# Kernel tuning notes

Hardware: AMD Instinct MI355X
Metric: run time of the kernel (lower is better)

Reference implementation:

```python
import jax, jax.numpy as jnp
import numpy as np


def _nn_idx(query, ref):
    """Index of nearest ref point for each query point.
    query: [B,N,3], ref: [B,M,3] -> idx [B,N] (int32).
    Squared distance via ||q||^2 - 2 q.r + ||r||^2 (matches cdist+top1).
    """
    d2 = (jnp.sum(query * query, axis=-1, keepdims=True)
          - 2.0 * jnp.einsum('bnd,bmd->bnm', query, ref)
          + jnp.sum(ref * ref, axis=-1)[:, None, :])
    return jnp.argmin(d2, axis=-1)


def setup_inputs() -> dict:
    key = jax.random.key(0)
    k1, k2, k3 = jax.random.split(key, 3)
    B, N, M = 1, 16384, 16384  # batch hard-coded to 1 in original loops
    pred = jax.random.normal(k1, (B, N, 3), dtype=jnp.float32)
    gt = jax.random.normal(k2, (B, M, 3), dtype=jnp.float32)
    weight = jax.random.uniform(k3, (1,), dtype=jnp.float32)
    return {"pred": pred, "gt": gt, "weight": weight}


def reference(pred, gt, weight):
    # get_mse_loss2: weighted bidirectional nearest-neighbor MSE.
    w = weight[0]
    # B2A: align each pred point to its nearest gt point
    idx = _nn_idx(pred, gt)                                   # [B,N]
    align_gt = jnp.take_along_axis(gt, idx[..., None], axis=1)  # [B,N,3]
    B2A = jnp.mean((pred - align_gt) ** 2)
    # A2B: align each gt point to its nearest pred point
    idx2 = _nn_idx(gt, pred)                                  # [B,M]
    align_out = jnp.take_along_axis(pred, idx2[..., None], axis=1)  # [B,M,3]
    A2B = jnp.mean((align_out - gt) ** 2)
    return B2A * w + A2B * (1.0 - w)
```

## Files before the change

### kernel.cpp

```cpp
#include <hip/hip_runtime.h>


#define NPTS   16384
#define QBLK   128
#define QCH    (NPTS / QBLK)
#define SSPLIT 4
#define RBLK   (NPTS / SSPLIT)
#define NB1    (2 * QCH * SSPLIT)

typedef __attribute__((ext_vector_type(8)))  __bf16 bf16x8;
typedef __attribute__((ext_vector_type(16))) float  floatx16;

union frag16 { __bf16 v[16]; uint4 q[2]; };

__device__ __forceinline__ float vmin16(floatx16 v) {
    float a = fminf(fminf(v[0], v[1]), v[2]);
    float b = fminf(fminf(v[3], v[4]), v[5]);
    float c = fminf(fminf(v[6], v[7]), v[8]);
    float d = fminf(fminf(v[9], v[10]), v[11]);
    float e = fminf(fminf(v[12], v[13]), fminf(v[14], v[15]));
    return fminf(fminf(fminf(a, b), fminf(c, d)), e);
}

__global__ __launch_bounds__(256) void prep_kernel(
    const float* __restrict__ pred, const float* __restrict__ gt,
    uint4* __restrict__ aform, uint4* __restrict__ bform,
    float* __restrict__ out)
{
    const int i = blockIdx.x * 256 + threadIdx.x;
    if (i == 0) out[0] = 0.0f;
    const int role = (i < NPTS) ? 0 : 1;
    const int p = i - role * NPTS;
    const float* __restrict__ src = role ? gt : pred;

    const float x = src[p * 3 + 0], y = src[p * 3 + 1], z = src[p * 3 + 2];
    const float nn = x * x + y * y + z * z;
    const __bf16 xh = (__bf16)x, yh = (__bf16)y, zh = (__bf16)z;
    const __bf16 xl = (__bf16)(x - (float)xh);
    const __bf16 yl = (__bf16)(y - (float)yh);
    const __bf16 zl = (__bf16)(z - (float)zh);
    const __bf16 nh = (__bf16)nn;
    const __bf16 nl = (__bf16)(nn - (float)nh);
    const __bf16 one = (__bf16)1.0f;

    frag16 A;
    A.v[0]  = (__bf16)(-2.0f * (float)xh); A.v[1]  = A.v[0];
    A.v[2]  = (__bf16)(-2.0f * (float)xl); A.v[3]  = A.v[2];
    A.v[4]  = (__bf16)(-2.0f * (float)yh); A.v[5]  = A.v[4];
    A.v[6]  = (__bf16)(-2.0f * (float)yl); A.v[7]  = A.v[6];
    A.v[8]  = (__bf16)(-2.0f * (float)zh); A.v[9]  = A.v[8];
    A.v[10] = (__bf16)(-2.0f * (float)zl); A.v[11] = A.v[10];
    A.v[12] = nh;  A.v[13] = nl;  A.v[14] = one;  A.v[15] = one;

    frag16 B;
    B.v[0] = xh;  B.v[1]  = xl;  B.v[2]  = xh;  B.v[3]  = xl;
    B.v[4] = yh;  B.v[5]  = yl;  B.v[6]  = yh;  B.v[7]  = yl;
    B.v[8] = zh;  B.v[9]  = zl;  B.v[10] = zh;  B.v[11] = zl;
    B.v[12] = one; B.v[13] = one; B.v[14] = nh;  B.v[15] = nl;

    uint4* da = aform + (size_t)role * (NPTS * 2)
              + ((p >> 5) * 64 + (p & 31));
    da[0]  = A.q[0];
    da[32] = A.q[1];
    uint4* db = bform + (size_t)role * (NPTS * 2) + p * 2;
    db[0] = B.q[0];
    db[1] = B.q[1];
}

__global__ __launch_bounds__(256) void nn_part_kernel(
    const uint4* __restrict__ aform, const uint4* __restrict__ bform,
    float* __restrict__ partial)
{
    const int bx   = blockIdx.x;
    const int dir  = bx >> 9;
    const int qc   = (bx & 511) >> 2;
    const int s    = bx & 3;
    const int tid  = threadIdx.x;
    const int lane = tid & 63;
    const int wave = tid >> 6;
    const int lid  = lane & 31;
    const int half = lane >> 5;

    const uint4* __restrict__ Aref = aform + (size_t)(dir ? 0 : 1) * (NPTS * 2);
    const uint4* __restrict__ Bqry = bform + (size_t)(dir ? 1 : 0) * (NPTS * 2);

    const int qbase = qc * QBLK + wave * 32;
    const bf16x8 bq = __builtin_bit_cast(bf16x8, Bqry[(qbase + lid) * 2 + half]);

    floatx16 zero;
#pragma unroll
    for (int k = 0; k < 16; ++k) zero[k] = 0.0f;
    floatx16 mnv;
#pragma unroll
    for (int k = 0; k < 16; ++k) mnv[k] = 3.4e38f;

    const uint4* gp = Aref + (size_t)s * (RBLK * 2) + half * 32 + lid;
#pragma unroll 4
    for (int t = 0; t < RBLK / 32; t += 2) {
        const bf16x8 a0 = __builtin_bit_cast(bf16x8, gp[t * 64]);
        const bf16x8 a1 = __builtin_bit_cast(bf16x8, gp[t * 64 + 64]);
        floatx16 d0 = __builtin_amdgcn_mfma_f32_32x32x16_bf16(a0, bq, zero, 0, 0, 0);
        floatx16 d1 = __builtin_amdgcn_mfma_f32_32x32x16_bf16(a1, bq, zero, 0, 0, 0);
#pragma unroll
        for (int k = 0; k < 16; ++k)
            mnv[k] = fminf(fminf(mnv[k], d0[k]), d1[k]);
    }

    float v = vmin16(mnv);
    v = fminf(v, __shfl_xor(v, 32));
    if (half == 0) {
        float* pout = partial + ((size_t)((dir * QCH + qc) * SSPLIT + s)) * QBLK
                    + wave * 32;
        pout[lid] = v;
    }
}

__global__ __launch_bounds__(QBLK) void nn_combine_kernel(
    const float* __restrict__ partial, const float* __restrict__ weight,
    float* __restrict__ out)
{
    const int b   = blockIdx.x;
    const int dir = b >> 7;
    const int qc  = b & 127;
    const int t   = threadIdx.x;

    const float* p = partial + ((size_t)((dir * QCH + qc) * SSPLIT)) * QBLK;
    float v = p[t];
#pragma unroll
    for (int s = 1; s < SSPLIT; ++s)
        v = fminf(v, p[s * QBLK + t]);

    for (int off = 32; off; off >>= 1) v += __shfl_down(v, off);
    __shared__ float ws[2];
    if ((t & 63) == 0) ws[t >> 6] = v;
    __syncthreads();
    if (t == 0) {
        const float sum = ws[0] + ws[1];
        const float wgt = weight[0];
        const float scale = (dir ? (1.0f - wgt) : wgt) / (3.0f * (float)NPTS);
        atomicAdd(out, sum * scale);
    }
}

extern "C" void kernel_launch(void* const* d_in, const int* in_sizes, int n_in,
                              void* d_out, int out_size, void* d_ws, size_t ws_size,
                              hipStream_t stream) {
    const float* pred   = (const float*)d_in[0];
    const float* gt     = (const float*)d_in[1];
    const float* weight = (const float*)d_in[2];

    float* partial = (float*)d_ws;
    uint4* aform = (uint4*)((char*)d_ws + (size_t)2 * QCH * SSPLIT * QBLK * 4);
    uint4* bform = aform + (size_t)2 * NPTS * 2;

    prep_kernel<<<2 * NPTS / 256, 256, 0, stream>>>(pred, gt, aform, bform,
                                                    (float*)d_out);
    nn_part_kernel<<<NB1, 256, 0, stream>>>(aform, bform, partial);
    nn_combine_kernel<<<2 * QCH, QBLK, 0, stream>>>(partial, weight, (float*)d_out);
}
```

Baseline: 92.68 us.

## Give each wave two query tiles and fuse MFMA with min3 in inline asm

Each wave now handles 64 query points with two B fragments, so every loaded reference A fragment feeds four MFMAs instead of two. The query block grows to 256 and the reference split to 8, which keeps the grid at 1024 blocks, and the combine kernel is resized to match. The MFMA-plus-min reduction is written in inline assembly using v_min3 on hard-coded clobbered registers v32–v63, with s_nop padding for the MFMA result hazard. The fixed nops may stall more than needed, and the hard register clobbers can constrain register allocation.

```diff
diff --git a/kernel.cpp b/kernel.cpp
--- a/kernel.cpp
+++ b/kernel.cpp
@@ -2,9 +2,9 @@
 
 
 #define NPTS   16384
-#define QBLK   128
+#define QBLK   256
 #define QCH    (NPTS / QBLK)
-#define SSPLIT 4
+#define SSPLIT 8
 #define RBLK   (NPTS / SSPLIT)
 #define NB1    (2 * QCH * SSPLIT)
 
@@ -12,15 +12,6 @@
 typedef __attribute__((ext_vector_type(16))) float  floatx16;
 
 union frag16 { __bf16 v[16]; uint4 q[2]; };
-
-__device__ __forceinline__ float vmin16(floatx16 v) {
-    float a = fminf(fminf(v[0], v[1]), v[2]);
-    float b = fminf(fminf(v[3], v[4]), v[5]);
-    float c = fminf(fminf(v[6], v[7]), v[8]);
-    float d = fminf(fminf(v[9], v[10]), v[11]);
-    float e = fminf(fminf(v[12], v[13]), fminf(v[14], v[15]));
-    return fminf(fminf(fminf(a, b), fminf(c, d)), e);
-}
 
 __global__ __launch_bounds__(256) void prep_kernel(
     const float* __restrict__ pred, const float* __restrict__ gt,
@@ -67,14 +58,47 @@
     db[1] = B.q[1];
 }
 
+#define MFMA_MIN_BLOCK(BQ, M)                                               \
+    asm volatile(                                                           \
+        "v_mfma_f32_32x32x16_bf16 v[32:47], %[A0], %[B], %[Z]\n\t"          \
+        "v_mfma_f32_32x32x16_bf16 v[48:63], %[A1], %[B], %[Z]\n\t"          \
+        "s_nop 7\n\ts_nop 7\n\ts_nop 7\n\ts_nop 7\n\t"                      \
+        "v_min3_f32 %[M0],  %[M0],  v32, v48\n\t"                           \
+        "v_min3_f32 %[M1],  %[M1],  v33, v49\n\t"                           \
+        "v_min3_f32 %[M2],  %[M2],  v34, v50\n\t"                           \
+        "v_min3_f32 %[M3],  %[M3],  v35, v51\n\t"                           \
+        "v_min3_f32 %[M4],  %[M4],  v36, v52\n\t"                           \
+        "v_min3_f32 %[M5],  %[M5],  v37, v53\n\t"                           \
+        "v_min3_f32 %[M6],  %[M6],  v38, v54\n\t"                           \
+        "v_min3_f32 %[M7],  %[M7],  v39, v55\n\t"                           \
+        "v_min3_f32 %[M8],  %[M8],  v40, v56\n\t"                           \
+        "v_min3_f32 %[M9],  %[M9],  v41, v57\n\t"                           \
+        "v_min3_f32 %[M10], %[M10], v42, v58\n\t"                           \
+        "v_min3_f32 %[M11], %[M11], v43, v59\n\t"                           \
+        "v_min3_f32 %[M12], %[M12], v44, v60\n\t"                           \
+        "v_min3_f32 %[M13], %[M13], v45, v61\n\t"                           \
+        "v_min3_f32 %[M14], %[M14], v46, v62\n\t"                           \
+        "v_min3_f32 %[M15], %[M15], v47, v63"                               \
+        : [M0] "+v"(M[0]),  [M1] "+v"(M[1]),  [M2] "+v"(M[2]),              \
+          [M3] "+v"(M[3]),  [M4] "+v"(M[4]),  [M5] "+v"(M[5]),              \
+          [M6] "+v"(M[6]),  [M7] "+v"(M[7]),  [M8] "+v"(M[8]),              \
+          [M9] "+v"(M[9]),  [M10] "+v"(M[10]), [M11] "+v"(M[11]),           \
+          [M12] "+v"(M[12]), [M13] "+v"(M[13]), [M14] "+v"(M[14]),          \
+          [M15] "+v"(M[15])                                                 \
+        : [A0] "v"(a0), [A1] "v"(a1), [B] "v"(BQ), [Z] "v"(zero)            \
+        : "v32", "v33", "v34", "v35", "v36", "v37", "v38", "v39",           \
+          "v40", "v41", "v42", "v43", "v44", "v45", "v46", "v47",           \
+          "v48", "v49", "v50", "v51", "v52", "v53", "v54", "v55",           \
+          "v56", "v57", "v58", "v59", "v60", "v61", "v62", "v63")
+
 __global__ __launch_bounds__(256) void nn_part_kernel(
     const uint4* __restrict__ aform, const uint4* __restrict__ bform,
     float* __restrict__ partial)
 {
     const int bx   = blockIdx.x;
     const int dir  = bx >> 9;
-    const int qc   = (bx & 511) >> 2;
-    const int s    = bx & 3;
+    const int qc   = (bx & 511) >> 3;
+    const int s    = bx & 7;
     const int tid  = threadIdx.x;
     const int lane = tid & 63;
     const int wave = tid >> 6;
@@ -84,44 +108,56 @@
     const uint4* __restrict__ Aref = aform + (size_t)(dir ? 0 : 1) * (NPTS * 2);
     const uint4* __restrict__ Bqry = bform + (size_t)(dir ? 1 : 0) * (NPTS * 2);
 
-    const int qbase = qc * QBLK + wave * 32;
-    const bf16x8 bq = __builtin_bit_cast(bf16x8, Bqry[(qbase + lid) * 2 + half]);
+    const int qbase = qc * QBLK + wave * 64;
+    const bf16x8 bq0 = __builtin_bit_cast(bf16x8, Bqry[(qbase + lid) * 2 + half]);
+    const bf16x8 bq1 = __builtin_bit_cast(bf16x8, Bqry[(qbase + 32 + lid) * 2 + half]);
 
     floatx16 zero;
 #pragma unroll
     for (int k = 0; k < 16; ++k) zero[k] = 0.0f;
-    floatx16 mnv;
+
+    float ma[16], mb[16];
 #pragma unroll
-    for (int k = 0; k < 16; ++k) mnv[k] = 3.4e38f;
+    for (int k = 0; k < 16; ++k) { ma[k] = 3.4e38f; mb[k] = 3.4e38f; }
 
     const uint4* gp = Aref + (size_t)s * (RBLK * 2) + half * 32 + lid;
-#pragma unroll 4
+#pragma unroll 2
     for (int t = 0; t < RBLK / 32; t += 2) {
         const bf16x8 a0 = __builtin_bit_cast(bf16x8, gp[t * 64]);
         const bf16x8 a1 = __builtin_bit_cast(bf16x8, gp[t * 64 + 64]);
-        floatx16 d0 = __builtin_amdgcn_mfma_f32_32x32x16_bf16(a0, bq, zero, 0, 0, 0);
-        floatx16 d1 = __builtin_amdgcn_mfma_f32_32x32x16_bf16(a1, bq, zero, 0, 0, 0);
-#pragma unroll
-        for (int k = 0; k < 16; ++k)
-            mnv[k] = fminf(fminf(mnv[k], d0[k]), d1[k]);
+        MFMA_MIN_BLOCK(bq0, ma);
+        MFMA_MIN_BLOCK(bq1, mb);
     }
 
-    float v = vmin16(mnv);
-    v = fminf(v, __shfl_xor(v, 32));
-    if (half == 0) {
-        float* pout = partial + ((size_t)((dir * QCH + qc) * SSPLIT + s)) * QBLK
-                    + wave * 32;
-        pout[lid] = v;
+    float* pout = partial + ((size_t)((dir * QCH + qc) * SSPLIT + s)) * QBLK
+                + wave * 64;
+    {
+        float a = fminf(fminf(ma[0], ma[1]), fminf(ma[2], ma[3]));
+        float b = fminf(fminf(ma[4], ma[5]), fminf(ma[6], ma[7]));
+        float c = fminf(fminf(ma[8], ma[9]), fminf(ma[10], ma[11]));
+        float d = fminf(fminf(ma[12], ma[13]), fminf(ma[14], ma[15]));
+        float v = fminf(fminf(a, b), fminf(c, d));
+        v = fminf(v, __shfl_xor(v, 32));
+        if (half == 0) pout[lid] = v;
+    }
+    {
+        float a = fminf(fminf(mb[0], mb[1]), fminf(mb[2], mb[3]));
+        float b = fminf(fminf(mb[4], mb[5]), fminf(mb[6], mb[7]));
+        float c = fminf(fminf(mb[8], mb[9]), fminf(mb[10], mb[11]));
+        float d = fminf(fminf(mb[12], mb[13]), fminf(mb[14], mb[15]));
+        float v = fminf(fminf(a, b), fminf(c, d));
+        v = fminf(v, __shfl_xor(v, 32));
+        if (half == 0) pout[32 + lid] = v;
     }
 }
 
-__global__ __launch_bounds__(QBLK) void nn_combine_kernel(
+__global__ __launch_bounds__(256) void nn_combine_kernel(
     const float* __restrict__ partial, const float* __restrict__ weight,
     float* __restrict__ out)
 {
     const int b   = blockIdx.x;
-    const int dir = b >> 7;
-    const int qc  = b & 127;
+    const int dir = b >> 6;
+    const int qc  = b & 63;
     const int t   = threadIdx.x;
 
     const float* p = partial + ((size_t)((dir * QCH + qc) * SSPLIT)) * QBLK;
@@ -131,11 +167,11 @@
         v = fminf(v, p[s * QBLK + t]);
 
     for (int off = 32; off; off >>= 1) v += __shfl_down(v, off);
-    __shared__ float ws[2];
+    __shared__ float ws[4];
     if ((t & 63) == 0) ws[t >> 6] = v;
     __syncthreads();
     if (t == 0) {
-        const float sum = ws[0] + ws[1];
+        const float sum = ws[0] + ws[1] + ws[2] + ws[3];
         const float wgt = weight[0];
         const float scale = (dir ? (1.0f - wgt) : wgt) / (3.0f * (float)NPTS);
         atomicAdd(out, sum * scale);
@@ -156,5 +192,5 @@
     prep_kernel<<<2 * NPTS / 256, 256, 0, stream>>>(pred, gt, aform, bform,
                                                     (float*)d_out);
     nn_part_kernel<<<NB1, 256, 0, stream>>>(aform, bform, partial);
-    nn_combine_kernel<<<2 * QCH, QBLK, 0, stream>>>(partial, weight, (float*)d_out);
+    nn_combine_kernel<<<2 * QCH, 256, 0, stream>>>(partial, weight, (float*)d_out);
 }
```

Result: faster. 81.32 us, median of 2 (-12.3%).
